# Kernel optimization log

Hardware: AMD Instinct MI355X
Metric: run time of the kernel (lower is better)

## Reference

```python
import jax, jax.numpy as jnp
import numpy as np

N_NODES = 100000
N_EDGES = 200000
N_FEAT = 300
HIDDEN = 300
NUM_GRAPHS = 2048
NUM_BOND_TYPE = 6
NUM_BOND_DIR = 3


def setup_inputs() -> dict:
    key = jax.random.key(0)
    ks = jax.random.split(key, 12)
    x = jax.random.normal(ks[0], (N_NODES, N_FEAT), dtype=jnp.float32)
    edge_index = jax.random.randint(ks[1], (2, N_EDGES), 0, N_NODES, dtype=jnp.int64)
    edge_attr = jax.random.randint(ks[2], (N_EDGES, 2), 0, NUM_BOND_DIR, dtype=jnp.int64)
    batch = jnp.sort(jax.random.randint(ks[3], (N_NODES,), 0, NUM_GRAPHS, dtype=jnp.int64))
    s = 1.0 / np.sqrt(N_FEAT)
    emb1 = jax.random.normal(ks[4], (NUM_BOND_TYPE, N_FEAT), dtype=jnp.float32) * s
    emb2 = jax.random.normal(ks[5], (NUM_BOND_DIR, N_FEAT), dtype=jnp.float32) * s
    W1 = jax.random.normal(ks[6], (N_FEAT, 2 * N_FEAT), dtype=jnp.float32) * s
    b1 = jnp.zeros((2 * N_FEAT,), dtype=jnp.float32)
    W2 = jax.random.normal(ks[7], (2 * N_FEAT, HIDDEN), dtype=jnp.float32) * (1.0 / np.sqrt(2 * N_FEAT))
    b2 = jnp.zeros((HIDDEN,), dtype=jnp.float32)
    Wfc = jax.random.normal(ks[8], (HIDDEN, HIDDEN), dtype=jnp.float32) * (1.0 / np.sqrt(HIDDEN))
    bfc = jnp.zeros((HIDDEN,), dtype=jnp.float32)
    return {"x": x, "edge_index": edge_index, "edge_attr": edge_attr, "batch": batch,
            "emb1": emb1, "emb2": emb2, "W1": W1, "b1": b1, "W2": W2, "b2": b2,
            "Wfc": Wfc, "bfc": bfc}


def reference(x, edge_index, edge_attr, batch, emb1, emb2, W1, b1, W2, b2, Wfc, bfc):
    n = x.shape[0]
    # add_self_loops(fill_value=0): append N self edges with zero edge_attr
    loop = jnp.arange(n, dtype=edge_index.dtype)
    src = jnp.concatenate([edge_index[0], loop])  # [E+N]
    dst = jnp.concatenate([edge_index[1], loop])
    ea = jnp.concatenate([edge_attr, jnp.zeros((n, 2), dtype=edge_attr.dtype)], axis=0)
    # edge embeddings (shared by both conv layers)
    edge_emb = emb1[ea[:, 0]] + emb2[ea[:, 1]]  # [E+N, F]

    def mlp(h):
        return jax.nn.relu(h @ W1 + b1) @ W2 + b2

    def gin(h):
        # message: x_j + edge_emb, scatter-add at target nodes, then shared MLP
        msg = h[src] + edge_emb
        aggr = jax.ops.segment_sum(msg, dst, num_segments=n)
        return mlp(aggr)

    h = jax.nn.relu(gin(x))
    h = jax.nn.relu(gin(h))
    # global_add_pool over graphs in batch
    g = jax.ops.segment_sum(h, batch, num_segments=NUM_GRAPHS)  # [G, H]
    return g @ Wfc + bfc
```

## Files before the change

kernel.cpp:

```cpp
#include <hip/hip_runtime.h>
#include <hip/hip_bf16.h>

#define NFEAT 300
#define KP 320
#define NGRAPH 2048
#define N1P 640
#define N2P 384
#define NTD 18
#define SCAN_B 2048

typedef __bf16 bf16x8 __attribute__((ext_vector_type(8)));
typedef float  f32x4  __attribute__((ext_vector_type(4)));
typedef unsigned short u16x8 __attribute__((ext_vector_type(8)));

__device__ __forceinline__ unsigned short f2b(float v) {
    union { float f; unsigned u; } x; x.f = v;
    unsigned r = x.u + 0x7fff + ((x.u >> 16) & 1);
    return (unsigned short)(r >> 16);
}
__device__ __forceinline__ float b2f(unsigned short u) {
    union { unsigned u; float f; } x; x.u = ((unsigned)u) << 16;
    return x.f;
}

#define GLD_LDS16(g, l)                                                        \
    __builtin_amdgcn_global_load_lds(                                          \
        (const __attribute__((address_space(1))) void*)(g),                    \
        (__attribute__((address_space(3))) void*)(l), 16, 0, 0)

__global__ __launch_bounds__(256) void k_embc(
    const float* __restrict__ emb1, const float* __restrict__ emb2,
    float* __restrict__ embc)
{
    int t = blockIdx.x * blockDim.x + threadIdx.x;
    if (t >= NTD * KP) return;
    int td = t / KP, c = t % KP;
    int t1 = td / 3, d = td % 3;
    embc[t] = (c < NFEAT) ? emb1[t1 * NFEAT + c] + emb2[d * NFEAT + c] : 0.f;
}

__global__ __launch_bounds__(256) void k_cvtX(
    const float* __restrict__ x, unsigned short* __restrict__ xb, int n, int Mpad)
{
    int idx = blockIdx.x * blockDim.x + threadIdx.x;
    if (idx >= Mpad * (KP / 8)) return;
    int row = idx / (KP / 8), c0 = (idx % (KP / 8)) * 8;
    unsigned short o[8];
#pragma unroll
    for (int j = 0; j < 8; ++j) {
        int col = c0 + j;
        float v = (row < n && col < NFEAT) ? x[(size_t)row * NFEAT + col] : 0.f;
        o[j] = f2b(v);
    }
    *(uint4*)&xb[(size_t)row * KP + c0] = *(uint4*)o;
}

__global__ __launch_bounds__(256) void k_zero(int* __restrict__ p, int n)
{
    int i = blockIdx.x * blockDim.x + threadIdx.x;
    if (i < n) p[i] = 0;
}

__global__ __launch_bounds__(256) void k_deg(
    const int* __restrict__ ei, int* __restrict__ deg, int E)
{
    int e = blockIdx.x * blockDim.x + threadIdx.x;
    if (e >= E) return;
    atomicAdd(&deg[ei[E + e]], 1);
}

__global__ __launch_bounds__(256) void k_scan1(
    const int* __restrict__ deg, int* __restrict__ offsets,
    int* __restrict__ bsum, int n)
{
    __shared__ int sh[256];
    int tid = threadIdx.x;
    int base = blockIdx.x * SCAN_B + tid * 8;
    int v[8], run = 0;
#pragma unroll
    for (int j = 0; j < 8; ++j) {
        int i = base + j;
        v[j] = (i < n) ? deg[i] : 0;
        run += v[j];
        v[j] = run;
    }
    sh[tid] = run;
    __syncthreads();
    for (int off = 1; off < 256; off <<= 1) {
        int t = (tid >= off) ? sh[tid - off] : 0;
        __syncthreads();
        sh[tid] += t;
        __syncthreads();
    }
    int excl = sh[tid] - run;
#pragma unroll
    for (int j = 0; j < 8; ++j) {
        int i = base + j;
        if (i < n) offsets[i + 1] = excl + v[j];
    }
    if (tid == 0) bsum[blockIdx.x] = sh[255];
}

__global__ void k_scan2(int* __restrict__ bsum, int nb, int* __restrict__ offsets)
{
    if (threadIdx.x == 0 && blockIdx.x == 0) {
        int run = 0;
        for (int b = 0; b < nb; ++b) { int t = bsum[b]; bsum[b] = run; run += t; }
        offsets[0] = 0;
    }
}

__global__ __launch_bounds__(256) void k_scan3(
    const int* __restrict__ deg, int* __restrict__ offsets,
    const int* __restrict__ bsum, int* __restrict__ cursor, int n)
{
    int i = blockIdx.x * blockDim.x + threadIdx.x;
    if (i >= n) return;
    int fin = offsets[i + 1] + bsum[i / SCAN_B];
    offsets[i + 1] = fin;
    cursor[i] = fin - deg[i];
}

__global__ __launch_bounds__(256) void k_fill(
    const int* __restrict__ ei, const int* __restrict__ ea,
    int* __restrict__ cursor, int* __restrict__ edgerec, int E)
{
    int e = blockIdx.x * blockDim.x + threadIdx.x;
    if (e >= E) return;
    int dst = ei[E + e];
    int pos = atomicAdd(&cursor[dst], 1);
    int src = ei[e];
    int td  = ea[2 * e] * 3 + ea[2 * e + 1];
    edgerec[pos] = src | (td << 20);
}

__global__ __launch_bounds__(256) void k_aggr(
    const unsigned short* __restrict__ h,
    const int* __restrict__ offsets, const int* __restrict__ edgerec,
    const float* __restrict__ embc,
    unsigned short* __restrict__ Ab, int n, int Mpad)
{
    int idx = blockIdx.x * blockDim.x + threadIdx.x;
    if (idx >= Mpad * (KP / 8)) return;
    int v = idx / (KP / 8), c0 = (idx % (KP / 8)) * 8;
    unsigned short* outp = &Ab[(size_t)v * KP + c0];
    if (v >= n) {
        *(uint4*)outp = make_uint4(0, 0, 0, 0);
        return;
    }
    float acc[8];
    u16x8 hv = *(const u16x8*)&h[(size_t)v * KP + c0];
    const float* e0 = embc + c0;
#pragma unroll
    for (int j = 0; j < 8; ++j) acc[j] = b2f(hv[j]) + e0[j];

    int beg = offsets[v], end = offsets[v + 1];
    for (int e = beg; e < end; ++e) {
        int rec = edgerec[e];
        int src = rec & 0xFFFFF;
        int td  = rec >> 20;
        u16x8 hs = *(const u16x8*)&h[(size_t)src * KP + c0];
        const float* ee = embc + td * KP + c0;
#pragma unroll
        for (int j = 0; j < 8; ++j) acc[j] += b2f(hs[j]) + ee[j];
    }
    unsigned short o[8];
#pragma unroll
    for (int j = 0; j < 8; ++j) o[j] = f2b(acc[j]);
    *(uint4*)outp = *(uint4*)o;
}

__global__ __launch_bounds__(256) void k_cvtW(
    const float* __restrict__ W, unsigned short* __restrict__ Wt,
    int rows, int cols, int Kpad, int Npad)
{
    int t = blockIdx.x * blockDim.x + threadIdx.x;
    if (t >= Npad * Kpad) return;
    int nn = t / Kpad, k = t % Kpad;
    float v = (k < rows && nn < cols) ? W[(size_t)k * cols + nn] : 0.f;
    Wt[t] = f2b(v);
}

__global__ __launch_bounds__(256) void k_gemm(
    const unsigned short* __restrict__ Ag, const unsigned short* __restrict__ Bg,
    const float* __restrict__ bias, int bias_n,
    unsigned short* __restrict__ C, int ldc, int store_cols,
    int K, int npass, int MT)
{
    __shared__ unsigned short smem[24576];

    int tid  = threadIdx.x;
    int lane = tid & 63, wave = tid >> 6;

    int l    = blockIdx.x;
    int xcd  = l & 7;
    int j    = l >> 3;
    int ncol = j % npass;
    int panel= (j / npass) * 8 + xcd;
    if (panel >= MT) return;
    int m0 = panel * 128;

    int wm = (wave >> 1) * 64, wn = (wave & 1) * 64;
    int fr = lane & 15, fq = lane >> 4;
    int colq = lane & 15, rq = (lane >> 4) * 4;

    const unsigned short* Abase = Ag + (size_t)m0 * K;
    const unsigned short* Bbase = Bg + (size_t)ncol * 128 * K;

    int c0 = tid, c1 = 256 + tid;
    size_t aoff0 = (size_t)(c0 >> 2) * K + 8 * ((c0 & 3) ^ ((c0 >> 3) & 3));
    size_t aoff1 = (size_t)(c1 >> 2) * K + 8 * ((c1 & 3) ^ ((c1 >> 3) & 3));

    int fswz = 8 * (fq ^ ((fr >> 1) & 3));

#define STAGEK(bi, kt_) do {                                                   \
        int _b  = (bi) * 8192;                                                 \
        int _k0 = (kt_) * 32;                                                  \
        GLD_LDS16(Abase + aoff0 + _k0, &smem[_b + c0 * 8]);                    \
        GLD_LDS16(Abase + aoff1 + _k0, &smem[_b + c1 * 8]);                    \
        GLD_LDS16(Bbase + aoff0 + _k0, &smem[_b + 4096 + c0 * 8]);             \
        GLD_LDS16(Bbase + aoff1 + _k0, &smem[_b + 4096 + c1 * 8]);             \
    } while (0)

#define SBAR() do {                                                            \
        __builtin_amdgcn_sched_barrier(0);                                     \
        __builtin_amdgcn_s_barrier();                                          \
        __builtin_amdgcn_sched_barrier(0);                                     \
    } while (0)

    f32x4 acc[4][4];
#pragma unroll
    for (int i = 0; i < 4; ++i)
#pragma unroll
        for (int jj = 0; jj < 4; ++jj)
            acc[i][jj] = (f32x4){0.f, 0.f, 0.f, 0.f};

    int NT = K >> 5;
    STAGEK(0, 0);
    STAGEK(1, 1);

    for (int kt = 0; kt < NT; ++kt) {
        int base = (kt % 3) * 8192;

        if (kt + 1 < NT) {
            asm volatile("s_waitcnt vmcnt(4)" ::: "memory");
        } else {
            asm volatile("s_waitcnt vmcnt(0)" ::: "memory");
        }
        SBAR();

        if (kt + 2 < NT) STAGEK((kt + 2) % 3, kt + 2);

        bf16x8 af[4], bfv[4];
#pragma unroll
        for (int i = 0; i < 4; ++i) {
            af[i]  = *(const bf16x8*)&smem[base + (wm + i * 16 + fr) * 32 + fswz];
            bfv[i] = *(const bf16x8*)&smem[base + 4096 + (wn + i * 16 + fr) * 32 + fswz];
        }
#pragma unroll
        for (int i = 0; i < 4; ++i)
#pragma unroll
            for (int jj = 0; jj < 4; ++jj)
                acc[i][jj] = __builtin_amdgcn_mfma_f32_16x16x32_bf16(
                    af[i], bfv[jj], acc[i][jj], 0, 0, 0);
    }
    __syncthreads();

#pragma unroll
    for (int ch = 0; ch < 2; ++ch) {
        if ((wn >> 6) == ch) {
#pragma unroll
            for (int jj = 0; jj < 4; ++jj) {
                int lc  = jj * 16 + colq;
                int col = ncol * 128 + wn + jj * 16 + colq;
                float bv = (col < bias_n) ? bias[col] : 0.f;
#pragma unroll
                for (int i = 0; i < 4; ++i) {
                    int rbase = wm + i * 16 + rq;
#pragma unroll
                    for (int r = 0; r < 4; ++r) {
                        float v = fmaxf(acc[i][jj][r] + bv, 0.f);
                        smem[(rbase + r) * 64 + lc] = f2b(v);
                    }
                }
            }
        }
        __syncthreads();
        int cbase = ncol * 128 + ch * 64;
        if (cbase < store_cols) {
#pragma unroll
            for (int i = 0; i < 4; ++i) {
                int idx = i * 256 + tid;
                int row = idx >> 3, c8 = idx & 7;
                *(uint4*)&C[(size_t)(m0 + row) * ldc + cbase + c8 * 8] =
                    *(uint4*)&smem[row * 64 + c8 * 8];
            }
        }
        __syncthreads();
    }
#undef STAGEK
#undef SBAR
}

__global__ __launch_bounds__(256) void k_pool(
    const unsigned short* __restrict__ H, const int* __restrict__ batch,
    float* __restrict__ g, int n)
{
    int gid = blockIdx.x;
    int lo = 0, hi = n;
    while (lo < hi) { int mid = (lo + hi) >> 1; if (batch[mid] < gid) lo = mid + 1; else hi = mid; }
    int start = lo;
    hi = n;
    while (lo < hi) { int mid = (lo + hi) >> 1; if (batch[mid] < gid + 1) lo = mid + 1; else hi = mid; }
    int end = lo;

    for (int f = threadIdx.x; f < NFEAT; f += blockDim.x) {
        float acc = 0.f;
        for (int v = start; v < end; ++v) acc += b2f(H[(size_t)v * KP + f]);
        g[(size_t)gid * NFEAT + f] = acc;
    }
}

__global__ __launch_bounds__(256) void k_final(
    const float* __restrict__ g, const float* __restrict__ Wfc,
    const float* __restrict__ bfc, float* __restrict__ out)
{
    int idx = blockIdx.x * blockDim.x + threadIdx.x;
    if (idx >= NGRAPH * NFEAT) return;
    int r = idx / NFEAT, c = idx % NFEAT;
    float acc = bfc[c];
    for (int k = 0; k < NFEAT; ++k)
        acc = fmaf(g[(size_t)r * NFEAT + k], Wfc[(size_t)k * NFEAT + c], acc);
    out[idx] = acc;
}

extern "C" void kernel_launch(void* const* d_in, const int* in_sizes, int n_in,
                              void* d_out, int out_size, void* d_ws, size_t ws_size,
                              hipStream_t stream)
{
    const float* x    = (const float*)d_in[0];
    const int*   ei   = (const int*)  d_in[1];
    const int*   ea   = (const int*)  d_in[2];
    const int*   batch= (const int*)  d_in[3];
    const float* emb1 = (const float*)d_in[4];
    const float* emb2 = (const float*)d_in[5];
    const float* W1   = (const float*)d_in[6];
    const float* b1   = (const float*)d_in[7];
    const float* W2   = (const float*)d_in[8];
    const float* b2   = (const float*)d_in[9];
    const float* Wfc  = (const float*)d_in[10];
    const float* bfc  = (const float*)d_in[11];
    float* out = (float*)d_out;

    int n = in_sizes[0] / NFEAT;
    int E = in_sizes[1] / 2;
    int MT   = (n + 127) / 128;
    int Mpad = MT * 128;
    int MT8  = ((MT + 7) / 8) * 8;

    char* p = (char*)d_ws;
    auto take = [&](size_t bytes) { char* r = p; p += (bytes + 255) & ~(size_t)255; return r; };
    unsigned short* T    = (unsigned short*)take((size_t)Mpad * N1P * 2);
    unsigned short* xb   = T;
    unsigned short* Ab   = (unsigned short*)take((size_t)Mpad * KP * 2);
    unsigned short* Hb   = (unsigned short*)take((size_t)Mpad * KP * 2);
    unsigned short* Wt1  = (unsigned short*)take((size_t)N1P * KP * 2);
    unsigned short* Wt2  = (unsigned short*)take((size_t)N2P * N1P * 2);
    float*          embc = (float*)take((size_t)NTD * KP * 4);
    float*          g    = (float*)take((size_t)NGRAPH * NFEAT * 4);
    int*            deg  = (int*)take((size_t)n * 4);
    int*            offs = (int*)take((size_t)(n + 1) * 4);
    int*            curs = (int*)take((size_t)n * 4);
    int*            erec = (int*)take((size_t)E * 4);
    int*            bsum = (int*)take(256 * 4);

    dim3 blk(256);
    int chunkThreads = Mpad * (KP / 8);
    int chunkBlocks  = (chunkThreads + 255) / 256;
    int nb = (n + SCAN_B - 1) / SCAN_B;

    k_cvtW<<<(N1P * KP + 255) / 256, blk, 0, stream>>>(W1, Wt1, NFEAT, 600, KP, N1P);
    k_cvtW<<<(N2P * N1P + 255) / 256, blk, 0, stream>>>(W2, Wt2, 600, NFEAT, N1P, N2P);
    k_embc<<<(NTD * KP + 255) / 256, blk, 0, stream>>>(emb1, emb2, embc);
    k_cvtX<<<chunkBlocks, blk, 0, stream>>>(x, xb, n, Mpad);

    k_zero <<<(n + 255) / 256, blk, 0, stream>>>(deg, n);
    k_deg  <<<(E + 255) / 256, blk, 0, stream>>>(ei, deg, E);
    k_scan1<<<nb, blk, 0, stream>>>(deg, offs, bsum, n);
    k_scan2<<<1, 64, 0, stream>>>(bsum, nb, offs);
    k_scan3<<<(n + 255) / 256, blk, 0, stream>>>(deg, offs, bsum, curs, n);
    k_fill <<<(E + 255) / 256, blk, 0, stream>>>(ei, ea, curs, erec, E);

    k_aggr<<<chunkBlocks, blk, 0, stream>>>(xb, offs, erec, embc, Ab, n, Mpad);
    k_gemm<<<MT8 * (N1P / 128), blk, 0, stream>>>(Ab, Wt1, b1, 600, T, N1P, N1P, KP, N1P / 128, MT);
    k_gemm<<<MT8 * (N2P / 128), blk, 0, stream>>>(T, Wt2, b2, NFEAT, Hb, KP, KP, N1P, N2P / 128, MT);

    k_aggr<<<chunkBlocks, blk, 0, stream>>>(Hb, offs, erec, embc, Ab, n, Mpad);
    k_gemm<<<MT8 * (N1P / 128), blk, 0, stream>>>(Ab, Wt1, b1, 600, T, N1P, N1P, KP, N1P / 128, MT);
    k_gemm<<<MT8 * (N2P / 128), blk, 0, stream>>>(T, Wt2, b2, NFEAT, Hb, KP, KP, N1P, N2P / 128, MT);

    k_pool <<<NGRAPH, blk, 0, stream>>>(Hb, batch, g, n);
    k_final<<<(NGRAPH * NFEAT + 255) / 256, blk, 0, stream>>>(g, Wfc, bfc, out);
}
```

Baseline: 697.0 us.

## Load GEMM B operand straight to registers and stage only A through LDS

```diff
diff --git a/kernel.cpp b/kernel.cpp
--- a/kernel.cpp
+++ b/kernel.cpp
@@ -187,7 +187,7 @@
     unsigned short* __restrict__ C, int ldc, int store_cols,
     int K, int npass, int MT)
 {
-    __shared__ unsigned short smem[24576];
+    __shared__ unsigned short smem[12288];
 
     int tid  = threadIdx.x;
     int lane = tid & 63, wave = tid >> 6;
@@ -206,6 +206,7 @@
 
     const unsigned short* Abase = Ag + (size_t)m0 * K;
     const unsigned short* Bbase = Bg + (size_t)ncol * 128 * K;
+    const unsigned short* Bp = Bbase + (size_t)(wn + fr) * K + fq * 8;
 
     int c0 = tid, c1 = 256 + tid;
     size_t aoff0 = (size_t)(c0 >> 2) * K + 8 * ((c0 & 3) ^ ((c0 >> 3) & 3));
@@ -214,12 +215,16 @@
     int fswz = 8 * (fq ^ ((fr >> 1) & 3));
 
 #define STAGEK(bi, kt_) do {                                                   \
-        int _b  = (bi) * 8192;                                                 \
+        int _b  = (bi) * 4096;                                                 \
         int _k0 = (kt_) * 32;                                                  \
         GLD_LDS16(Abase + aoff0 + _k0, &smem[_b + c0 * 8]);                    \
         GLD_LDS16(Abase + aoff1 + _k0, &smem[_b + c1 * 8]);                    \
-        GLD_LDS16(Bbase + aoff0 + _k0, &smem[_b + 4096 + c0 * 8]);             \
-        GLD_LDS16(Bbase + aoff1 + _k0, &smem[_b + 4096 + c1 * 8]);             \
+    } while (0)
+
+#define BLOAD(dst, kt_) do {                                                   \
+        _Pragma("unroll")                                                      \
+        for (int _jj = 0; _jj < 4; ++_jj)                                      \
+            dst[_jj] = *(const bf16x8*)&Bp[(size_t)_jj * 16 * K + (kt_) * 32]; \
     } while (0)
 
 #define SBAR() do {                                                            \
@@ -228,6 +233,27 @@
         __builtin_amdgcn_sched_barrier(0);                                     \
     } while (0)
 
+#define GITER(kt_, BC, BN) do {                                                \
+        int _base = ((kt_) % 3) * 4096;                                        \
+        if ((kt_) + 1 < NT) { asm volatile("s_waitcnt vmcnt(2)" ::: "memory"); } \
+        else                { asm volatile("s_waitcnt vmcnt(0)" ::: "memory"); } \
+        SBAR();                                                                \
+        if ((kt_) + 1 < NT) BLOAD(BN, (kt_) + 1);                              \
+        __builtin_amdgcn_sched_barrier(0);                                     \
+        if ((kt_) + 2 < NT) STAGEK(((kt_) + 2) % 3, (kt_) + 2);                \
+        __builtin_amdgcn_sched_barrier(0);                                     \
+        bf16x8 _af[4];                                                         \
+        _Pragma("unroll")                                                      \
+        for (int _i = 0; _i < 4; ++_i)                                         \
+            _af[_i] = *(const bf16x8*)&smem[_base + (wm + _i * 16 + fr) * 32 + fswz]; \
+        _Pragma("unroll")                                                      \
+        for (int _i = 0; _i < 4; ++_i)                                         \
+            _Pragma("unroll")                                                  \
+            for (int _jj = 0; _jj < 4; ++_jj)                                  \
+                acc[_i][_jj] = __builtin_amdgcn_mfma_f32_16x16x32_bf16(        \
+                    _af[_i], BC[_jj], acc[_i][_jj], 0, 0, 0);                  \
+    } while (0)
+
     f32x4 acc[4][4];
 #pragma unroll
     for (int i = 0; i < 4; ++i)
@@ -236,33 +262,17 @@
             acc[i][jj] = (f32x4){0.f, 0.f, 0.f, 0.f};
 
     int NT = K >> 5;
+    bf16x8 bc[4], bn[4];
+
+    BLOAD(bc, 0);
+    __builtin_amdgcn_sched_barrier(0);
     STAGEK(0, 0);
     STAGEK(1, 1);
-
-    for (int kt = 0; kt < NT; ++kt) {
-        int base = (kt % 3) * 8192;
-
-        if (kt + 1 < NT) {
-            asm volatile("s_waitcnt vmcnt(4)" ::: "memory");
-        } else {
-            asm volatile("s_waitcnt vmcnt(0)" ::: "memory");
-        }
-        SBAR();
-
-        if (kt + 2 < NT) STAGEK((kt + 2) % 3, kt + 2);
-
-        bf16x8 af[4], bfv[4];
-#pragma unroll
-        for (int i = 0; i < 4; ++i) {
-            af[i]  = *(const bf16x8*)&smem[base + (wm + i * 16 + fr) * 32 + fswz];
-            bfv[i] = *(const bf16x8*)&smem[base + 4096 + (wn + i * 16 + fr) * 32 + fswz];
-        }
-#pragma unroll
-        for (int i = 0; i < 4; ++i)
-#pragma unroll
-            for (int jj = 0; jj < 4; ++jj)
-                acc[i][jj] = __builtin_amdgcn_mfma_f32_16x16x32_bf16(
-                    af[i], bfv[jj], acc[i][jj], 0, 0, 0);
+    __builtin_amdgcn_sched_barrier(0);
+
+    for (int kt = 0; kt < NT; kt += 2) {
+        GITER(kt,     bc, bn);
+        GITER(kt + 1, bn, bc);
     }
     __syncthreads();
 
@@ -298,8 +308,10 @@
         }
         __syncthreads();
     }
+#undef GITER
+#undef SBAR
+#undef BLOAD
 #undef STAGEK
-#undef SBAR
 }
 
 __global__ __launch_bounds__(256) void k_pool(
```

After: 867.7 us. +24.5%, slower.
